# Kernel optimization log

Hardware: AMD Instinct MI355X
Metric: run time of the kernel (lower is better)

The kernel has to match this reference:

```python
import jax, jax.numpy as jnp
import numpy as np

VOCAB, EMB, HID, TAGS, T = 200000, 128, 256, 17, 8192


def setup_inputs() -> dict:
    key = jax.random.key(0)
    ks = jax.random.split(key, 8)
    s = 0.05
    return {
        "sentence": jax.random.randint(ks[0], (1, T), 0, VOCAB),
        "embedding": jax.random.normal(ks[1], (VOCAB, EMB), jnp.float32) * s,
        "W_ih": jax.random.normal(ks[2], (4 * HID, EMB), jnp.float32) * s,
        "W_hh": jax.random.normal(ks[3], (4 * HID, HID), jnp.float32) * s,
        "b_ih": jax.random.normal(ks[4], (4 * HID,), jnp.float32) * s,
        "b_hh": jax.random.normal(ks[5], (4 * HID,), jnp.float32) * s,
        "W_out": jax.random.normal(ks[6], (TAGS, HID), jnp.float32) * s,
        "b_out": jax.random.normal(ks[7], (TAGS,), jnp.float32) * s,
    }


def reference(sentence, embedding, W_ih, W_hh, b_ih, b_hh, W_out, b_out):
    # batch must be 1 (as implied by the original view-based reshapes)
    tokens = sentence[0]                       # [T]
    embeds = embedding[tokens]                 # [T, EMB]  (memory-bound gather)
    # precompute input projections for all timesteps (torch gate order: i,f,g,o)
    xg = embeds @ W_ih.T + b_ih + b_hh         # [T, 4H]
    H = W_hh.shape[1]

    def step(carry, xg_t):
        h, c = carry
        gates = xg_t + h @ W_hh.T              # [4H]
        i = jax.nn.sigmoid(gates[0 * H:1 * H])
        f = jax.nn.sigmoid(gates[1 * H:2 * H])
        g = jnp.tanh(gates[2 * H:3 * H])
        o = jax.nn.sigmoid(gates[3 * H:4 * H])
        c = f * c + i * g
        h = o * jnp.tanh(c)
        return (h, c), h

    h0 = jnp.zeros((H,), embeds.dtype)
    c0 = jnp.zeros((H,), embeds.dtype)
    _, lstm_out = jax.lax.scan(step, (h0, c0), xg)   # [T, H]
    tag_space = lstm_out @ W_out.T + b_out           # [T, TAGS]
    return jax.nn.log_softmax(tag_space, axis=1)
```

## Files before the change

kernel.cpp:

```cpp
#include <hip/hip_runtime.h>
#include <stdint.h>

#define TT    8192
#define EMBD  128
#define HID   256
#define G4    1024
#define NTAGS 17
#define NBLK  16
#define SH    16
#define QW    68

typedef unsigned int u32;

__device__ __forceinline__ float sigf(float x) { return 1.f / (1.f + __expf(-x)); }
__device__ __forceinline__ float tanhf_fast(float x) {
    x = fminf(15.f, fmaxf(-15.f, x));
    float a = __expf(2.f * x);
    return (a - 1.f) / (a + 1.f);
}

__global__ __launch_bounds__(256) void xg_kernel(
    const int* __restrict__ tok, const float* __restrict__ emb,
    const float* __restrict__ Wih, const float* __restrict__ bih,
    const float* __restrict__ bhh, float* __restrict__ xg)
{
    __shared__ __align__(16) float es[4][EMBD];
    const int tid = threadIdx.x;
    const int t0  = blockIdx.x * 4;

    for (int p = tid; p < 4 * EMBD; p += 256) {
        const int tt = p >> 7, k = p & 127;
        es[tt][k] = emb[(long)tok[t0 + tt] * EMBD + k];
    }
    __syncthreads();

#pragma unroll
    for (int q = 0; q < 4; ++q) {
        const int j = q * 256 + tid;
        const float4* wr = (const float4*)(Wih + (long)j * EMBD);
        float a0 = 0.f, a1 = 0.f, a2 = 0.f, a3 = 0.f;
#pragma unroll 8
        for (int k4 = 0; k4 < EMBD / 4; ++k4) {
            const float4 w  = wr[k4];
            const float4 e0 = ((const float4*)es[0])[k4];
            const float4 e1 = ((const float4*)es[1])[k4];
            const float4 e2 = ((const float4*)es[2])[k4];
            const float4 e3 = ((const float4*)es[3])[k4];
            a0 += w.x*e0.x + w.y*e0.y + w.z*e0.z + w.w*e0.w;
            a1 += w.x*e1.x + w.y*e1.y + w.z*e1.z + w.w*e1.w;
            a2 += w.x*e2.x + w.y*e2.y + w.z*e2.z + w.w*e2.w;
            a3 += w.x*e3.x + w.y*e3.y + w.z*e3.z + w.w*e3.w;
        }
        const float bb = bih[j] + bhh[j];
        xg[(long)(t0 + 0) * G4 + j] = a0 + bb;
        xg[(long)(t0 + 1) * G4 + j] = a1 + bb;
        xg[(long)(t0 + 2) * G4 + j] = a2 + bb;
        xg[(long)(t0 + 3) * G4 + j] = a3 + bb;
    }
}

__global__ __launch_bounds__(256) void lstm_kernel(
    const float* __restrict__ Whh, const float* __restrict__ xg,
    u32* __restrict__ hx)
{
    const int tid = threadIdx.x;
    const int b   = blockIdx.x;
    const int w   = tid >> 6;
    const int L   = tid & 63;
    const int g   = L >> 4;
    const int l15 = L & 15;
    const int hi  = l15 >> 2;
    const int q   = L & 3;
    const int row = g * HID + b * SH + w * 4 + hi;

    float4 wv[16];
    const float4* wsrc = (const float4*)(Whh + (long)row * HID + q * 64);
#pragma unroll
    for (int j = 0; j < 16; ++j) wv[j] = wsrc[j];

    __shared__ __align__(16) float hlds[2][4 * QW];
    for (int i = tid; i < 4 * QW; i += 256) hlds[0][i] = 0.f;
    __syncthreads();

    float c_reg = 0.f;
    const bool leader = (g == 0) && (q == 0);
    const int  gidx   = b * SH + w * 4 + hi;
    const int  myslot = (tid >> 6) * QW + (tid & 63);

    const float* xgp = xg + row;

    float xg0 = xgp[0];
    float xg1 = xgp[G4];

    auto step = [&](int s, float xgv) {
        const int cur = s & 1;
        const float* hb = &hlds[cur][q * QW];
        float p0 = 0.f, p1 = 0.f, p2 = 0.f, p3 = 0.f;
#pragma unroll
        for (int j = 0; j < 16; ++j) {
            const float4 hv = *(const float4*)(hb + j * 4);
            p0 += wv[j].x * hv.x; p1 += wv[j].y * hv.y;
            p2 += wv[j].z * hv.z; p3 += wv[j].w * hv.w;
        }
        float p = (p0 + p1) + (p2 + p3);
        p += __shfl_xor(p, 1, 64);
        p += __shfl_xor(p, 2, 64);
        const float pre = p + xgv;
        const float vf = __shfl(pre, 16 + l15, 64);
        const float vg = __shfl(pre, 32 + l15, 64);
        const float vo = __shfl(pre, 48 + l15, 64);
        if (leader) {
            const float i_ = sigf(pre);
            const float f_ = sigf(vf);
            const float g_ = tanhf_fast(vg);
            const float o_ = sigf(vo);
            c_reg = f_ * c_reg + i_ * g_;
            const float hn = o_ * tanhf_fast(c_reg);
            u32 hb32 = __float_as_uint(hn);
            u32 rb   = (hb32 + 0x7FFFu + ((hb32 >> 16) & 1u)) >> 16;
            __hip_atomic_store(&hx[(long)(s + 1) * HID + gidx],
                               ((u32)(s + 1) << 16) | rb,
                               __ATOMIC_RELAXED, __HIP_MEMORY_SCOPE_AGENT);
            hlds[cur ^ 1][(gidx >> 6) * QW + (gidx & 63)] =
                __uint_as_float(rb << 16);
        }
        if ((tid >> 4) != b) {
            const u32 want = (u32)(s + 1) << 16;
            u32* wp = &hx[(long)(s + 1) * HID + tid];
            u32 u;
            do { u = __hip_atomic_load(wp, __ATOMIC_RELAXED,
                                       __HIP_MEMORY_SCOPE_AGENT); }
            while ((u & 0xFFFF0000u) != want);
            hlds[cur ^ 1][myslot] = __uint_as_float(u << 16);
        }
        __syncthreads();
    };

    for (int s = 0; s < TT; s += 2) {
        const float xgn0 = xgp[(long)(s + 2) * G4];
        step(s, xg0);
        const float xgn1 = xgp[(long)(s + 3) * G4];
        step(s + 1, xg1);
        xg0 = xgn0; xg1 = xgn1;
    }
}

__global__ __launch_bounds__(64) void out_kernel(
    const u32* __restrict__ hx, const float* __restrict__ Wout,
    const float* __restrict__ bout, float* __restrict__ out)
{
    const int t   = blockIdx.x;
    const int tid = threadIdx.x;
    __shared__ __align__(16) float hs[HID];
    __shared__ float lg[NTAGS];

    const uint4 uu = ((const uint4*)(hx + (long)(t + 1) * HID))[tid];
    hs[tid * 4 + 0] = __uint_as_float(uu.x << 16);
    hs[tid * 4 + 1] = __uint_as_float(uu.y << 16);
    hs[tid * 4 + 2] = __uint_as_float(uu.z << 16);
    hs[tid * 4 + 3] = __uint_as_float(uu.w << 16);
    __syncthreads();

    if (tid < NTAGS) {
        const float4* wr = (const float4*)(Wout + (long)tid * HID);
        float p = 0.f;
#pragma unroll 8
        for (int qq = 0; qq < HID / 4; ++qq) {
            const float4 w = wr[qq];
            const float4 h = ((const float4*)hs)[qq];
            p += w.x*h.x + w.y*h.y + w.z*h.z + w.w*h.w;
        }
        lg[tid] = p + bout[tid];
    }
    __syncthreads();

    if (tid < NTAGS) {
        float m = -1e30f;
        for (int gg = 0; gg < NTAGS; ++gg) m = fmaxf(m, lg[gg]);
        float ss = 0.f;
        for (int gg = 0; gg < NTAGS; ++gg) ss += __expf(lg[gg] - m);
        out[(long)t * NTAGS + tid] = lg[tid] - (m + __logf(ss));
    }
}

extern "C" void kernel_launch(void* const* d_in, const int* in_sizes, int n_in,
                              void* d_out, int out_size, void* d_ws, size_t ws_size,
                              hipStream_t stream)
{
    const int*   tok  = (const int*)  d_in[0];
    const float* emb  = (const float*)d_in[1];
    const float* Wih  = (const float*)d_in[2];
    const float* Whh  = (const float*)d_in[3];
    const float* bih  = (const float*)d_in[4];
    const float* bhh  = (const float*)d_in[5];
    const float* Wout = (const float*)d_in[6];
    const float* bout = (const float*)d_in[7];
    float* out = (float*)d_out;

    char* ws = (char*)d_ws;
    float* xg = (float*)(ws);
    u32*   hx = (u32*)  (ws + 33554432UL);

    xg_kernel  <<<TT / 4, 256, 0, stream>>>(tok, emb, Wih, bih, bhh, xg);
    lstm_kernel<<<NBLK,   256, 0, stream>>>(Whh, xg, hx);
    out_kernel <<<TT,     64,  0, stream>>>(hx, Wout, bout, out);
}
```

Baseline: 18.46 ms.

## Co-locate LSTM blocks on one XCD and poll h via sc0 loads

The recurrent kernel now launches 256 blocks. Each block reads its XCC id from a hardware register, and the first XCC to gather 16 blocks wins; all other blocks exit. Cross-block h exchange then stays within one XCD's L2, using sc0 stores and loads instead of agent-scope atomics. A fallback agent-scope mirror buffer is polled every 64 spins so the wait cannot hang. This relies on 16 blocks being co-resident on one XCC and on inline asm cache semantics, and it adds launch and election overhead.

```diff
diff --git a/kernel.cpp b/kernel.cpp
--- a/kernel.cpp
+++ b/kernel.cpp
@@ -9,6 +9,7 @@
 #define NBLK  16
 #define SH    16
 #define QW    68
+#define REG_GRID 256
 
 typedef unsigned int u32;
 
@@ -19,14 +20,31 @@
     return (a - 1.f) / (a + 1.f);
 }
 
+__device__ __forceinline__ u32 load_u32_sc0(const u32* p) {
+    u32 v;
+    asm volatile("global_load_dword %0, %1, off sc0\n\ts_waitcnt vmcnt(0)"
+                 : "=v"(v) : "v"(p) : "memory");
+    return v;
+}
+__device__ __forceinline__ void store_u32_sc0(u32* p, u32 v) {
+    asm volatile("global_store_dword %0, %1, off sc0" :: "v"(p), "v"(v) : "memory");
+}
+
 __global__ __launch_bounds__(256) void xg_kernel(
     const int* __restrict__ tok, const float* __restrict__ emb,
     const float* __restrict__ Wih, const float* __restrict__ bih,
-    const float* __restrict__ bhh, float* __restrict__ xg)
+    const float* __restrict__ bhh, float* __restrict__ xg,
+    int* __restrict__ pool, int* __restrict__ winner, u32* __restrict__ hx2)
 {
     __shared__ __align__(16) float es[4][EMBD];
     const int tid = threadIdx.x;
     const int t0  = blockIdx.x * 4;
+
+    if (blockIdx.x == 0) {
+        if (tid < 16) pool[tid] = 0;
+        if (tid == 16) *winner = -1;
+        if (tid < 2 * HID + 32) hx2[tid] = 0u;
+    }
 
     for (int p = tid; p < 4 * EMBD; p += 256) {
         const int tt = p >> 7, k = p & 127;
@@ -59,12 +77,31 @@
     }
 }
 
-__global__ __launch_bounds__(256) void lstm_kernel(
+__global__ __launch_bounds__(256, 2) void lstm_kernel(
     const float* __restrict__ Whh, const float* __restrict__ xg,
-    u32* __restrict__ hx)
+    u32* __restrict__ hx, u32* __restrict__ hx2,
+    int* __restrict__ pool, int* __restrict__ winner)
 {
     const int tid = threadIdx.x;
-    const int b   = blockIdx.x;
+    __shared__ int s_b;
+    if (tid == 0) {
+        const u32 xcc = __builtin_amdgcn_s_getreg(20 | (31 << 11)) & 0xFu;
+        int b = -1;
+        const int slot = atomicAdd(&pool[xcc], 1);
+        if (slot < NBLK) {
+            if (slot == NBLK - 1) atomicCAS(winner, -1, (int)xcc);
+            int w;
+            while ((w = __hip_atomic_load(winner, __ATOMIC_RELAXED,
+                                          __HIP_MEMORY_SCOPE_AGENT)) == -1)
+                __builtin_amdgcn_s_sleep(8);
+            if (w == (int)xcc) b = slot;
+        }
+        s_b = b;
+    }
+    __syncthreads();
+    const int b = s_b;
+    if (b < 0) return;
+
     const int w   = tid >> 6;
     const int L   = tid & 63;
     const int g   = L >> 4;
@@ -88,10 +125,8 @@
     const int  myslot = (tid >> 6) * QW + (tid & 63);
 
     const float* xgp = xg + row;
-
     float xg0 = xgp[0];
     float xg1 = xgp[G4];
-
     auto step = [&](int s, float xgv) {
         const int cur = s & 1;
         const float* hb = &hlds[cur][q * QW];
@@ -116,21 +151,29 @@
             const float o_ = sigf(vo);
             c_reg = f_ * c_reg + i_ * g_;
             const float hn = o_ * tanhf_fast(c_reg);
-            u32 hb32 = __float_as_uint(hn);
-            u32 rb   = (hb32 + 0x7FFFu + ((hb32 >> 16) & 1u)) >> 16;
-            __hip_atomic_store(&hx[(long)(s + 1) * HID + gidx],
-                               ((u32)(s + 1) << 16) | rb,
+            const u32 hb32 = __float_as_uint(hn);
+            const u32 rb   = (hb32 + 0x7FFFu + ((hb32 >> 16) & 1u)) >> 16;
+            const u32 word = ((u32)(s + 1) << 16) | rb;
+            store_u32_sc0(&hx[(long)(s + 1) * HID + gidx], word);
+            __hip_atomic_store(&hx2[((s + 1) & 1) * HID + gidx], word,
                                __ATOMIC_RELAXED, __HIP_MEMORY_SCOPE_AGENT);
             hlds[cur ^ 1][(gidx >> 6) * QW + (gidx & 63)] =
                 __uint_as_float(rb << 16);
         }
         if ((tid >> 4) != b) {
             const u32 want = (u32)(s + 1) << 16;
-            u32* wp = &hx[(long)(s + 1) * HID + tid];
-            u32 u;
-            do { u = __hip_atomic_load(wp, __ATOMIC_RELAXED,
-                                       __HIP_MEMORY_SCOPE_AGENT); }
-            while ((u & 0xFFFF0000u) != want);
+            u32* wp  = &hx[(long)(s + 1) * HID + tid];
+            u32* wp2 = &hx2[((s + 1) & 1) * HID + tid];
+            u32 u; int spins = 0;
+            for (;;) {
+                u = load_u32_sc0(wp);
+                if ((u & 0xFFFF0000u) == want) break;
+                if ((++spins & 63) == 0) {
+                    u = __hip_atomic_load(wp2, __ATOMIC_RELAXED,
+                                          __HIP_MEMORY_SCOPE_AGENT);
+                    if ((u & 0xFFFF0000u) == want) break;
+                }
+            }
             hlds[cur ^ 1][myslot] = __uint_as_float(u << 16);
         }
         __syncthreads();
@@ -198,10 +241,14 @@
     float* out = (float*)d_out;
 
     char* ws = (char*)d_ws;
-    float* xg = (float*)(ws);
-    u32*   hx = (u32*)  (ws + 33554432UL);
-
-    xg_kernel  <<<TT / 4, 256, 0, stream>>>(tok, emb, Wih, bih, bhh, xg);
-    lstm_kernel<<<NBLK,   256, 0, stream>>>(Whh, xg, hx);
-    out_kernel <<<TT,     64,  0, stream>>>(hx, Wout, bout, out);
-}
+    float* xg     = (float*)(ws);
+    u32*   hx     = (u32*)  (ws + 33554432UL);
+    u32*   hx2    = (u32*)  (ws + 33554432UL + 8389632UL);
+    int*   pool   = (int*)  (ws + 33554432UL + 8389632UL + 2176UL);
+    int*   winner = (int*)  (ws + 33554432UL + 8389632UL + 2176UL + 64UL);
+
+    xg_kernel  <<<TT / 4,   256, 0, stream>>>(tok, emb, Wih, bih, bhh, xg,
+                                              pool, winner, hx2);
+    lstm_kernel<<<REG_GRID, 256, 0, stream>>>(Whh, xg, hx, hx2, pool, winner);
+    out_kernel <<<TT,       64,  0, stream>>>(hx, Wout, bout, out);
+}
```

New measurement: 69.48 ms. +276.3%, slower.
